# Kernel tuning notes

Hardware: AMD Instinct MI355X
Metric: run time of the kernel (lower is better)

The kernel has to match this reference:

```python
import jax, jax.numpy as jnp
import numpy as np

HEADS = 8
DIM_HEAD = 64
WINDOW = 256
CAUSAL = True


def _sliding_window_mask(seq_len: int, window: int, causal: bool) -> jnp.ndarray:
    i = jnp.arange(seq_len)[:, None]
    j = jnp.arange(seq_len)[None, :]
    # attend iff i - window + 1 <= j <= i + window - 1 (end_pos exclusive)
    mask = (j >= i - window + 1) & (j <= i + window - 1)
    if causal:
        mask = mask & (j <= i)
    return mask  # (S, S) bool


def setup_inputs() -> dict:
    key = jax.random.key(0)
    k1, k2, k3 = jax.random.split(key, 3)
    dim = 512
    inner = HEADS * DIM_HEAD
    x = jax.random.normal(k1, (2, 2048, dim), dtype=jnp.float32)
    W_qkv = jax.random.normal(k2, (dim, 3 * inner), dtype=jnp.float32) * 0.02
    W_out = jax.random.normal(k3, (inner, dim), dtype=jnp.float32) * 0.02
    return {"x": x, "W_qkv": W_qkv, "W_out": W_out}


def reference(x, W_qkv, W_out):
    B, S, D = x.shape
    H, Dh = HEADS, DIM_HEAD
    scale = Dh ** (-0.5)
    qkv = x @ W_qkv  # (B, S, 3*H*Dh)
    q, k, v = jnp.split(qkv, 3, axis=-1)
    q = q.reshape(B, S, H, Dh).transpose(0, 2, 1, 3)  # (B, H, S, Dh)
    k = k.reshape(B, S, H, Dh).transpose(0, 2, 1, 3)
    v = v.reshape(B, S, H, Dh).transpose(0, 2, 1, 3)
    scores = jnp.einsum('bhid,bhjd->bhij', q, k) * scale
    mask = _sliding_window_mask(S, WINDOW, CAUSAL)
    mask_value = -jnp.finfo(scores.dtype).max
    scores = jnp.where(mask[None, None, :, :], scores, mask_value)
    attn = jax.nn.softmax(scores, axis=-1)  # (B, H, S, S)
    out = jnp.einsum('bhij,bhjd->bhid', attn, v)
    out = out.transpose(0, 2, 1, 3).reshape(B, S, H * Dh)
    out = out @ W_out  # (B, S, D)
    return (out, attn)
```

## Files before the change

kernel.cpp:

```cpp
#include <hip/hip_runtime.h>
#include <hip/hip_bf16.h>

typedef __bf16 bf16x8 __attribute__((ext_vector_type(8)));
typedef __bf16 bf16x4 __attribute__((ext_vector_type(4)));
typedef float f32x4 __attribute__((ext_vector_type(4)));

#define MFMA16(a,b,c) __builtin_amdgcn_mfma_f32_16x16x32_bf16(a, b, c, 0, 0, 0)

__device__ inline void fill_attn_rows(float* __restrict__ attn, int rowStart, int rowEnd,
                                      int tid) {
  const f32x4 z4 = {0.f, 0.f, 0.f, 0.f};
  for (int g = rowStart; g < rowEnd; g++) {
    const int bh = g >> 11, i = g & 2047;
    const int qt = i >> 6;
    const int lo = qt >= 4 ? (qt - 4) << 6 : 0;
    const int hi = (qt + 1) << 6;
    float* rp = attn + ((size_t)bh << 22) + ((size_t)i << 11);
    for (int j = tid << 2; j < lo; j += 1024)
      __builtin_nontemporal_store(z4, reinterpret_cast<f32x4*>(rp + j));
    for (int j = hi + (tid << 2); j < 2048; j += 1024)
      __builtin_nontemporal_store(z4, reinterpret_cast<f32x4*>(rp + j));
  }
}

__device__ inline void fill_block_chunk(float* __restrict__ attn, int fillStart, int fillEnd,
                                        int fid, int nfill, int tid) {
  const int total = fillEnd - fillStart;
  const int per = (total + nfill - 1) / nfill;
  const int myStart = fillStart + fid * per;
  int myEnd = myStart + per;
  if (myEnd > fillEnd) myEnd = fillEnd;
  if (myStart < myEnd) fill_attn_rows(attn, myStart, myEnd, tid);
}

__device__ inline void transpose_body(const float* __restrict__ in, __bf16* __restrict__ out,
                                      int R, int C, int tile, int tid, float (*t)[65]) {
  const int tilesC = C >> 6;
  const int tc = tile % tilesC, tr = tile / tilesC;
  const int r0 = tr << 6, c0 = tc << 6;
  const int ri = tid >> 2, cq = (tid & 3) << 4;
#pragma unroll
  for (int e = 0; e < 16; e += 4) {
    float4 v = *reinterpret_cast<const float4*>(&in[(size_t)(r0 + ri) * C + c0 + cq + e]);
    t[ri][cq + e]     = v.x;
    t[ri][cq + e + 1] = v.y;
    t[ri][cq + e + 2] = v.z;
    t[ri][cq + e + 3] = v.w;
  }
  __syncthreads();
  const int co = tid >> 2, rq = (tid & 3) << 4;
  __attribute__((aligned(16))) __bf16 buf[16];
#pragma unroll
  for (int e = 0; e < 16; e++) buf[e] = (__bf16)t[rq + e][co];
  *reinterpret_cast<bf16x8*>(&out[(size_t)(c0 + co) * R + r0 + rq])     = *reinterpret_cast<bf16x8*>(&buf[0]);
  *reinterpret_cast<bf16x8*>(&out[(size_t)(c0 + co) * R + r0 + rq + 8]) = *reinterpret_cast<bf16x8*>(&buf[8]);
}

__global__ __launch_bounds__(256) void prep(const float* __restrict__ Wqkv,
                                            const float* __restrict__ Wout,
                                            __bf16* __restrict__ Wqt,
                                            __bf16* __restrict__ Wot) {
  __shared__ float t[64][65];
  const int bid = blockIdx.x, tid = threadIdx.x;
  if (bid < 192) transpose_body(Wqkv, Wqt, 512, 1536, bid, tid, t);
  else           transpose_body(Wout, Wot, 512, 512, bid - 192, tid, t);
}

template <typename AT, typename OT>
__global__ __launch_bounds__(256) void gemm_bt(const AT* __restrict__ A,
                                               const __bf16* __restrict__ Bt,
                                               OT* __restrict__ C, int M, int N, int K,
                                               float* __restrict__ fillAttn,
                                               int fillStart, int fillEnd, int gxCompute) {
  __shared__ __bf16 As[128][72];
  __shared__ __bf16 Bs[128][72];
  const int tid = threadIdx.x;

  if ((int)blockIdx.x >= gxCompute) {
    const int nfx = gridDim.x - gxCompute;
    const int fid = (blockIdx.x - gxCompute) + nfx * blockIdx.y;
    fill_block_chunk(fillAttn, fillStart, fillEnd, fid, nfx * gridDim.y, tid);
    return;
  }

  const int wave = tid >> 6, lane = tid & 63;
  const int c = lane & 15, q4 = lane >> 4;
  const int bm = blockIdx.y << 7, bn = blockIdx.x << 7;
  const int wm = (wave >> 1) << 6, wn = (wave & 1) << 6;
  f32x4 acc[4][4];
#pragma unroll
  for (int m = 0; m < 4; m++)
#pragma unroll
    for (int n = 0; n < 4; n++)
#pragma unroll
      for (int e = 0; e < 4; e++) acc[m][n][e] = 0.f;

  const int srow = tid >> 1, scol = (tid & 1) << 5;
  bf16x8 av[4], bv[4];

  auto loadA = [&](int k0) {
    const AT* ag = A + (size_t)(bm + srow) * K + k0 + scol;
    if constexpr (sizeof(AT) == 4) {
#pragma unroll
      for (int r = 0; r < 4; r++) {
        float4 lo = *reinterpret_cast<const float4*>(ag + r * 8);
        float4 hi = *reinterpret_cast<const float4*>(ag + r * 8 + 4);
        bf16x8 v;
        v[0] = (__bf16)lo.x; v[1] = (__bf16)lo.y; v[2] = (__bf16)lo.z; v[3] = (__bf16)lo.w;
        v[4] = (__bf16)hi.x; v[5] = (__bf16)hi.y; v[6] = (__bf16)hi.z; v[7] = (__bf16)hi.w;
        av[r] = v;
      }
    } else {
#pragma unroll
      for (int r = 0; r < 4; r++) av[r] = *reinterpret_cast<const bf16x8*>(ag + r * 8);
    }
  };
  auto loadB = [&](int k0) {
    const __bf16* bg = Bt + (size_t)(bn + srow) * K + k0 + scol;
#pragma unroll
    for (int r = 0; r < 4; r++) bv[r] = *reinterpret_cast<const bf16x8*>(bg + r * 8);
  };

  loadA(0); loadB(0);
  for (int k0 = 0; k0 < K; k0 += 64) {
    __syncthreads();
#pragma unroll
    for (int r = 0; r < 4; r++) *reinterpret_cast<bf16x8*>(&As[srow][scol + r * 8]) = av[r];
#pragma unroll
    for (int r = 0; r < 4; r++) *reinterpret_cast<bf16x8*>(&Bs[srow][scol + r * 8]) = bv[r];
    __syncthreads();
    if (k0 + 64 < K) { loadA(k0 + 64); loadB(k0 + 64); }
#pragma unroll
    for (int ks = 0; ks < 2; ks++) {
      const int kk = ks * 32 + q4 * 8;
      bf16x8 af[4], bfv[4];
#pragma unroll
      for (int m = 0; m < 4; m++) af[m] = *reinterpret_cast<const bf16x8*>(&As[wm + m * 16 + c][kk]);
#pragma unroll
      for (int n = 0; n < 4; n++) bfv[n] = *reinterpret_cast<const bf16x8*>(&Bs[wn + n * 16 + c][kk]);
#pragma unroll
      for (int m = 0; m < 4; m++)
#pragma unroll
        for (int n = 0; n < 4; n++) acc[m][n] = MFMA16(af[m], bfv[n], acc[m][n]);
    }
  }
#pragma unroll
  for (int m = 0; m < 4; m++)
#pragma unroll
    for (int n = 0; n < 4; n++)
#pragma unroll
      for (int r2 = 0; r2 < 4; r2++) {
        const int row = bm + wm + m * 16 + q4 * 4 + r2;
        const int col = bn + wn + n * 16 + c;
        C[(size_t)row * N + col] = (OT)acc[m][n][r2];
      }
}

__global__ __launch_bounds__(256) void attn_fused(const __bf16* __restrict__ QKV,
                                                  float* __restrict__ attn,
                                                  __bf16* __restrict__ AO) {
  __shared__ __bf16 Qs[64][72];
  __shared__ __bf16 Ks[2][64][72];
  __shared__ __bf16 Ps[2][64][72];
  __shared__ float red[4][64];
  __shared__ float rowstat[64];
  const int tid = threadIdx.x;

  if (blockIdx.x >= 32) {
    const int fid = (blockIdx.x - 32) + (gridDim.x - 32) * blockIdx.y;
    fill_block_chunk(attn, 16000, 24000, fid, (gridDim.x - 32) * gridDim.y, tid);
    return;
  }

  const int qt = blockIdx.x, bh = blockIdx.y;
  const int b = bh >> 3, h = bh & 7;
  const int qi0 = qt << 6;
  const int wave = tid >> 6, lane = tid & 63;
  const int c = lane & 15, q4 = lane >> 4;
  const int base = b * 2048;
  const int r = tid >> 2, qq = (tid & 3) << 4;

  {
    const __bf16* src = QKV + (size_t)(base + qi0 + r) * 1536 + h * 64 + qq;
    *reinterpret_cast<bf16x8*>(&Qs[r][qq]) = *reinterpret_cast<const bf16x8*>(src);
    *reinterpret_cast<bf16x8*>(&Qs[r][qq + 8]) = *reinterpret_cast<const bf16x8*>(src + 8);
  }

  f32x4 acc[5][4];
#pragma unroll
  for (int t = 0; t < 5; t++)
#pragma unroll
    for (int m = 0; m < 4; m++)
#pragma unroll
      for (int e = 0; e < 4; e++) acc[t][m][e] = 0.f;

  const int tfirst = qt >= 4 ? 0 : 4 - qt;
  bf16x8 kv0, kv1;
  {
    const __bf16* s = QKV + (size_t)(base + ((qt - 4 + tfirst) << 6) + r) * 1536 + 512 + h * 64 + qq;
    kv0 = *reinterpret_cast<const bf16x8*>(s);
    kv1 = *reinterpret_cast<const bf16x8*>(s + 8);
  }
  int cur = 0;
#pragma unroll
  for (int t = 0; t < 5; t++) {
    if (qt - 4 + t < 0) continue;
    *reinterpret_cast<bf16x8*>(&Ks[cur][r][qq]) = kv0;
    *reinterpret_cast<bf16x8*>(&Ks[cur][r][qq + 8]) = kv1;
    if (t < 4) {
      const __bf16* s = QKV + (size_t)(base + ((qt - 3 + t) << 6) + r) * 1536 + 512 + h * 64 + qq;
      kv0 = *reinterpret_cast<const bf16x8*>(s);
      kv1 = *reinterpret_cast<const bf16x8*>(s + 8);
    }
    __syncthreads();
#pragma unroll
    for (int ks = 0; ks < 2; ks++) {
      const int kk = ks * 32 + q4 * 8;
      bf16x8 bfr = *reinterpret_cast<const bf16x8*>(&Ks[cur][wave * 16 + c][kk]);
#pragma unroll
      for (int m = 0; m < 4; m++) {
        bf16x8 afr = *reinterpret_cast<const bf16x8*>(&Qs[m * 16 + c][kk]);
        acc[t][m] = MFMA16(afr, bfr, acc[t][m]);
      }
    }
    cur ^= 1;
  }

  const float scale = 0.125f;
#pragma unroll
  for (int t = 0; t < 5; t++) {
    const int jb = ((qt - 4 + t) << 6) + wave * 16 + c;
#pragma unroll
    for (int m = 0; m < 4; m++)
#pragma unroll
      for (int r2 = 0; r2 < 4; r2++) {
        const int ig = qi0 + m * 16 + q4 * 4 + r2;
        const bool valid = (jb >= 0) && (jb <= ig) && (jb >= ig - 255);
        acc[t][m][r2] = valid ? acc[t][m][r2] * scale : -1e30f;
      }
  }

  float pm[16];
#pragma unroll
  for (int m = 0; m < 4; m++)
#pragma unroll
    for (int r2 = 0; r2 < 4; r2++) {
      float v = acc[0][m][r2];
#pragma unroll
      for (int t = 1; t < 5; t++) v = fmaxf(v, acc[t][m][r2]);
      pm[m * 4 + r2] = v;
    }
#pragma unroll
  for (int off = 8; off >= 1; off >>= 1)
#pragma unroll
    for (int i = 0; i < 16; i++) pm[i] = fmaxf(pm[i], __shfl_xor(pm[i], off, 64));
  if (c == 0) {
#pragma unroll
    for (int m = 0; m < 4; m++)
#pragma unroll
      for (int r2 = 0; r2 < 4; r2++) red[wave][m * 16 + q4 * 4 + r2] = pm[m * 4 + r2];
  }
  __syncthreads();
  if (tid < 64)
    rowstat[tid] = fmaxf(fmaxf(red[0][tid], red[1][tid]), fmaxf(red[2][tid], red[3][tid]));
  __syncthreads();

  float rmax[16], ps[16];
#pragma unroll
  for (int m = 0; m < 4; m++)
#pragma unroll
    for (int r2 = 0; r2 < 4; r2++) {
      rmax[m * 4 + r2] = rowstat[m * 16 + q4 * 4 + r2];
      ps[m * 4 + r2] = 0.f;
    }
#pragma unroll
  for (int t = 0; t < 5; t++)
#pragma unroll
    for (int m = 0; m < 4; m++)
#pragma unroll
      for (int r2 = 0; r2 < 4; r2++) {
        float p = __expf(acc[t][m][r2] - rmax[m * 4 + r2]);
        acc[t][m][r2] = p;
        ps[m * 4 + r2] += p;
      }
#pragma unroll
  for (int off = 8; off >= 1; off >>= 1)
#pragma unroll
    for (int i = 0; i < 16; i++) ps[i] += __shfl_xor(ps[i], off, 64);
  if (c == 0) {
#pragma unroll
    for (int m = 0; m < 4; m++)
#pragma unroll
      for (int r2 = 0; r2 < 4; r2++) red[wave][m * 16 + q4 * 4 + r2] = ps[m * 4 + r2];
  }
  __syncthreads();
  if (tid < 64) rowstat[tid] = red[0][tid] + red[1][tid] + red[2][tid] + red[3][tid];
  __syncthreads();

#pragma unroll
  for (int m = 0; m < 4; m++)
#pragma unroll
    for (int r2 = 0; r2 < 4; r2++) {
      const float rinv = 1.0f / rowstat[m * 16 + q4 * 4 + r2];
#pragma unroll
      for (int t = 0; t < 5; t++) acc[t][m][r2] *= rinv;
    }

  f32x4 o[4];
#pragma unroll
  for (int n = 0; n < 4; n++)
#pragma unroll
    for (int e = 0; e < 4; e++) o[n][e] = 0.f;

  const int jv = tid >> 2, dqa = tid & 3;
  bf16x8 vr0, vr1;
  {
    const __bf16* s = QKV + (size_t)(base + ((qt - 4 + tfirst) << 6) + jv) * 1536 + 1024 + h * 64;
    vr0 = *reinterpret_cast<const bf16x8*>(s + dqa * 8);
    vr1 = *reinterpret_cast<const bf16x8*>(s + (dqa + 4) * 8);
  }
  int pcur = 0;
#pragma unroll
  for (int t = 0; t < 5; t++) {
    if (qt - 4 + t < 0) continue;
#pragma unroll
    for (int m = 0; m < 4; m++)
#pragma unroll
      for (int r2 = 0; r2 < 4; r2++)
        Ps[pcur][m * 16 + q4 * 4 + r2][wave * 16 + c] = (__bf16)acc[t][m][r2];
#pragma unroll
    for (int e = 0; e < 8; e++) {
      Ks[pcur][dqa * 8 + e][jv] = vr0[e];
      Ks[pcur][(dqa + 4) * 8 + e][jv] = vr1[e];
    }
    if (t < 4) {
      const __bf16* s = QKV + (size_t)(base + ((qt - 3 + t) << 6) + jv) * 1536 + 1024 + h * 64;
      vr0 = *reinterpret_cast<const bf16x8*>(s + dqa * 8);
      vr1 = *reinterpret_cast<const bf16x8*>(s + (dqa + 4) * 8);
    }
    __syncthreads();
#pragma unroll
    for (int ks = 0; ks < 2; ks++) {
      const int kk = ks * 32 + q4 * 8;
      bf16x8 af = *reinterpret_cast<const bf16x8*>(&Ps[pcur][wave * 16 + c][kk]);
#pragma unroll
      for (int n = 0; n < 4; n++) {
        bf16x8 bfr = *reinterpret_cast<const bf16x8*>(&Ks[pcur][n * 16 + c][kk]);
        o[n] = MFMA16(af, bfr, o[n]);
      }
    }
    pcur ^= 1;
  }

#pragma unroll
  for (int n = 0; n < 4; n++)
#pragma unroll
    for (int r2 = 0; r2 < 4; r2++) {
      const int i = qi0 + wave * 16 + q4 * 4 + r2;
      const int d = n * 16 + c;
      AO[(size_t)(base + i) * 512 + h * 64 + d] = (__bf16)o[n][r2];
    }

  float* arow = attn + ((size_t)bh << 22);
#pragma unroll
  for (int t = 0; t < 5; t++) {
    const int jt0 = (qt - 4 + t) << 6;
    if (jt0 < 0) continue;
    const int jb = jt0 + wave * 16 + c;
#pragma unroll
    for (int m = 0; m < 4; m++)
#pragma unroll
      for (int r2 = 0; r2 < 4; r2++) {
        const int ig = qi0 + m * 16 + q4 * 4 + r2;
        arow[(size_t)ig * 2048 + jb] = acc[t][m][r2];
      }
  }
}

extern "C" void kernel_launch(void* const* d_in, const int* in_sizes, int n_in,
                              void* d_out, int out_size, void* d_ws, size_t ws_size,
                              hipStream_t stream) {
  const float* x = (const float*)d_in[0];
  const float* Wqkv = (const float*)d_in[1];
  const float* Wout = (const float*)d_in[2];
  float* out = (float*)d_out;
  float* attn = out + (size_t)2 * 2048 * 512;

  char* ws = (char*)d_ws;
  __bf16* Wqt  = (__bf16*)(ws);
  __bf16* Wot  = (__bf16*)(ws + 1572864);
  __bf16* QKVb = (__bf16*)(ws + 1572864 + 524288);
  __bf16* AOb  = (__bf16*)(ws + 1572864 + 524288 + 12582912);

  prep<<<256, 256, 0, stream>>>(Wqkv, Wout, Wqt, Wot);

  gemm_bt<float, __bf16><<<dim3(24, 32), 256, 0, stream>>>(x, Wqt, QKVb, 4096, 1536, 512,
                                                           attn, 0, 16000, 12);

  attn_fused<<<dim3(48, 16), 256, 0, stream>>>(QKVb, attn, AOb);

  gemm_bt<__bf16, float><<<dim3(12, 32), 256, 0, stream>>>(AOb, Wot, out, 4096, 512, 512,
                                                           attn, 24000, 32768, 4);
}
```

Measured before the change: 88.66 us.

## Replace static zero-fill partition with atomic work-stealing shared by compute blocks

```diff
diff --git a/kernel.cpp b/kernel.cpp
--- a/kernel.cpp
+++ b/kernel.cpp
@@ -23,14 +23,21 @@
   }
 }
 
-__device__ inline void fill_block_chunk(float* __restrict__ attn, int fillStart, int fillEnd,
-                                        int fid, int nfill, int tid) {
-  const int total = fillEnd - fillStart;
-  const int per = (total + nfill - 1) / nfill;
-  const int myStart = fillStart + fid * per;
-  int myEnd = myStart + per;
-  if (myEnd > fillEnd) myEnd = fillEnd;
-  if (myStart < myEnd) fill_attn_rows(attn, myStart, myEnd, tid);
+__device__ inline void fill_steal(float* __restrict__ attn, int rowStart, int rowEnd,
+                                  unsigned int* __restrict__ cnt, int tid) {
+  __shared__ int sIdx;
+  const int nChunks = (rowEnd - rowStart + 7) >> 3;
+  for (;;) {
+    if (tid == 0) sIdx = (int)atomicAdd(cnt, 1u);
+    __syncthreads();
+    const int idx = sIdx;
+    __syncthreads();
+    if (idx >= nChunks) return;
+    const int r0 = rowStart + (idx << 3);
+    int r1 = r0 + 8;
+    if (r1 > rowEnd) r1 = rowEnd;
+    fill_attn_rows(attn, r0, r1, tid);
+  }
 }
 
 __device__ inline void transpose_body(const float* __restrict__ in, __bf16* __restrict__ out,
@@ -71,15 +78,15 @@
                                                const __bf16* __restrict__ Bt,
                                                OT* __restrict__ C, int M, int N, int K,
                                                float* __restrict__ fillAttn,
-                                               int fillStart, int fillEnd, int gxCompute) {
+                                               int fillStart, int fillEnd,
+                                               unsigned int* __restrict__ cnt,
+                                               int gxCompute) {
   __shared__ __bf16 As[128][72];
   __shared__ __bf16 Bs[128][72];
   const int tid = threadIdx.x;
 
   if ((int)blockIdx.x >= gxCompute) {
-    const int nfx = gridDim.x - gxCompute;
-    const int fid = (blockIdx.x - gxCompute) + nfx * blockIdx.y;
-    fill_block_chunk(fillAttn, fillStart, fillEnd, fid, nfx * gridDim.y, tid);
+    fill_steal(fillAttn, fillStart, fillEnd, cnt, tid);
     return;
   }
 
@@ -154,11 +161,14 @@
         const int col = bn + wn + n * 16 + c;
         C[(size_t)row * N + col] = (OT)acc[m][n][r2];
       }
+
+  fill_steal(fillAttn, fillStart, fillEnd, cnt, tid);
 }
 
 __global__ __launch_bounds__(256) void attn_fused(const __bf16* __restrict__ QKV,
                                                   float* __restrict__ attn,
-                                                  __bf16* __restrict__ AO) {
+                                                  __bf16* __restrict__ AO,
+                                                  unsigned int* __restrict__ cnt) {
   __shared__ __bf16 Qs[64][72];
   __shared__ __bf16 Ks[2][64][72];
   __shared__ __bf16 Ps[2][64][72];
@@ -167,8 +177,7 @@
   const int tid = threadIdx.x;
 
   if (blockIdx.x >= 32) {
-    const int fid = (blockIdx.x - 32) + (gridDim.x - 32) * blockIdx.y;
-    fill_block_chunk(attn, 16000, 24000, fid, (gridDim.x - 32) * gridDim.y, tid);
+    fill_steal(attn, 16000, 24000, cnt, tid);
     return;
   }
 
@@ -375,6 +384,8 @@
         arow[(size_t)ig * 2048 + jb] = acc[t][m][r2];
       }
   }
+
+  fill_steal(attn, 16000, 24000, cnt, tid);
 }
 
 extern "C" void kernel_launch(void* const* d_in, const int* in_sizes, int n_in,
@@ -391,14 +402,17 @@
   __bf16* Wot  = (__bf16*)(ws + 1572864);
   __bf16* QKVb = (__bf16*)(ws + 1572864 + 524288);
   __bf16* AOb  = (__bf16*)(ws + 1572864 + 524288 + 12582912);
+  unsigned int* cnt = (unsigned int*)(ws + 1572864 + 524288 + 12582912 + 4194304);
+
+  hipMemsetAsync(cnt, 0, 64, stream);
 
   prep<<<256, 256, 0, stream>>>(Wqkv, Wout, Wqt, Wot);
 
   gemm_bt<float, __bf16><<<dim3(24, 32), 256, 0, stream>>>(x, Wqt, QKVb, 4096, 1536, 512,
-                                                           attn, 0, 16000, 12);
-
-  attn_fused<<<dim3(48, 16), 256, 0, stream>>>(QKVb, attn, AOb);
+                                                           attn, 0, 16000, cnt + 0, 12);
+
+  attn_fused<<<dim3(48, 16), 256, 0, stream>>>(QKVb, attn, AOb, cnt + 1);
 
   gemm_bt<__bf16, float><<<dim3(12, 32), 256, 0, stream>>>(AOb, Wot, out, 4096, 512, 512,
-                                                           attn, 24000, 32768, 4);
-}
+                                                           attn, 24000, 32768, cnt + 2, 4);
+}
```

Result: slower. 107.3 us (+21.0%).
